# Kernel optimization log

Hardware: AMD Instinct MI355X
Metric: run time of the kernel (lower is better)

The kernel has to match this reference:

```python
import jax, jax.numpy as jnp
import numpy as np

EMBED = 256; HEADS = 8; LEVELS = 1; POINTS = 4; QUEUE = 2
HB = 200; WB = 200; NQ = HB * WB; BS = 1


def bilinear_sample(img, grid, h, w):
    # img: (BH, D, h*w) flattened feature map; grid: (BH, N, 2) in [-1, 1]
    # torch.grid_sample(align_corners=False, padding_mode='zeros') semantics
    gx, gy = grid[..., 0], grid[..., 1]
    x = (gx + 1.0) * (w * 0.5) - 0.5
    y = (gy + 1.0) * (h * 0.5) - 0.5
    x0 = jnp.floor(x); y0 = jnp.floor(y)
    lx = x - x0; ly = y - y0
    x0i = x0.astype(jnp.int32); y0i = y0.astype(jnp.int32)

    def corner(xi, yi, wgt):
        valid = ((xi >= 0) & (xi < w) & (yi >= 0) & (yi < h)).astype(img.dtype)
        idx = jnp.clip(yi, 0, h - 1) * w + jnp.clip(xi, 0, w - 1)  # (BH, N)
        vals = jax.vmap(lambda im, ix: im[:, ix])(img, idx)  # (BH, D, N)
        return vals * (wgt * valid)[:, None, :]

    return (corner(x0i, y0i, (1 - lx) * (1 - ly))
            + corner(x0i + 1, y0i, lx * (1 - ly))
            + corner(x0i, y0i + 1, (1 - lx) * ly)
            + corner(x0i + 1, y0i + 1, lx * ly))


def ms_deform_attn(value, shapes, loc, aw):
    # value: (B, Nv, H, D); loc: (B, nq, H, L, P, 2); aw: (B, nq, H, L, P)
    B, Nv, H, D = value.shape
    nq = loc.shape[1]; P = loc.shape[4]
    grids = 2.0 * loc - 1.0
    start = 0
    per_level = []
    for l in range(shapes.shape[0]):
        h, w = int(shapes[l, 0]), int(shapes[l, 1])
        vl = value[:, start:start + h * w].reshape(B, h, w, H, D)
        vl = vl.transpose(0, 3, 4, 1, 2).reshape(B * H, D, h * w)
        g = grids[:, :, :, l].transpose(0, 2, 1, 3, 4).reshape(B * H, nq * P, 2)
        samp = bilinear_sample(vl, g, h, w).reshape(B, H, D, nq, P)
        per_level.append(samp)
        start += h * w
    sampled = jnp.stack(per_level, axis=4)  # (B, H, D, nq, L, P)
    w_ = aw.transpose(0, 2, 1, 3, 4)[:, :, None]  # (B, H, 1, nq, L, P)
    out = (sampled * w_).sum(axis=(-1, -2))  # (B, H, D, nq)
    return out.reshape(B, H * D, nq).transpose(0, 2, 1)  # (B, nq, E)


def setup_inputs():
    key = jax.random.key(0)
    ks = jax.random.split(key, 10)
    s = 0.02
    n_off = QUEUE * HEADS * LEVELS * POINTS * 2
    n_aw = QUEUE * HEADS * LEVELS * POINTS
    return {
        "query": jax.random.normal(ks[0], (BS, NQ, EMBED), jnp.float32),
        "query_pos": jax.random.normal(ks[1], (BS, NQ, EMBED), jnp.float32),
        "value": jax.random.normal(ks[2], (BS * QUEUE, NQ, EMBED), jnp.float32),
        "reference_points": jax.random.uniform(ks[3], (BS * QUEUE, NQ, LEVELS, 2), jnp.float32),
        "spatial_shapes": jnp.array([[HB, WB]], dtype=jnp.int32),
        "W_off": jax.random.normal(ks[4], (EMBED * QUEUE, n_off), jnp.float32) * s,
        "b_off": jnp.zeros((n_off,), jnp.float32),
        "W_attn": jax.random.normal(ks[5], (EMBED * QUEUE, n_aw), jnp.float32) * s,
        "b_attn": jnp.zeros((n_aw,), jnp.float32),
        "W_val": jax.random.normal(ks[6], (EMBED, EMBED), jnp.float32) * s,
        "b_val": jnp.zeros((EMBED,), jnp.float32),
        "W_out": jax.random.normal(ks[7], (EMBED, EMBED), jnp.float32) * s,
        "b_out": jnp.zeros((EMBED,), jnp.float32),
    }


def reference(query, query_pos, value, reference_points, spatial_shapes,
              W_off, b_off, W_attn, b_attn, W_val, b_val, W_out, b_out):
    shapes = np.asarray(spatial_shapes)  # static level shapes
    bs, nq, E = query.shape
    identity = query
    q = query + query_pos
    # temporal query: concat current-frame value with query
    q2 = jnp.concatenate([value[:bs], q], axis=-1)  # (bs, nq, 2E)
    v = value @ W_val + b_val  # (bs*2, nv, E)
    nv = v.shape[1]
    v = v.reshape(bs * QUEUE, nv, HEADS, E // HEADS)
    off = (q2 @ W_off + b_off).reshape(bs, nq, HEADS, QUEUE, LEVELS, POINTS, 2)
    aw = (q2 @ W_attn + b_attn).reshape(bs, nq, HEADS, QUEUE, LEVELS * POINTS)
    aw = jax.nn.softmax(aw, axis=-1).reshape(bs, nq, HEADS, QUEUE, LEVELS, POINTS)
    aw = aw.transpose(0, 3, 1, 2, 4, 5).reshape(bs * QUEUE, nq, HEADS, LEVELS, POINTS)
    off = off.transpose(0, 3, 1, 2, 4, 5, 6).reshape(bs * QUEUE, nq, HEADS, LEVELS, POINTS, 2)
    # normalized sampling locations: (bs*2, nq, H, L, P, 2)
    normalizer = jnp.stack([spatial_shapes[..., 1], spatial_shapes[..., 0]], -1).astype(jnp.float32)
    loc = reference_points[:, :, None, :, None, :] + off / normalizer[None, None, None, :, None, :]
    out = ms_deform_attn(v, shapes, loc, aw)  # (bs*2, nq, E)
    # average over the BEV queue (current + history)
    out = out.transpose(1, 2, 0).reshape(nq, E, bs, QUEUE).mean(-1).transpose(2, 0, 1)
    out = out @ W_out + b_out
    return out + identity
```

## Files before the change

kernel.cpp:

```cpp
#include <hip/hip_runtime.h>
#include <math.h>

#define NQ    40000
#define EMB   256
#define NHEAD 8
#define HDIM  32
#define HB    200
#define WB    200
#define NCOL  192
#define HPIX  2560000

typedef __attribute__((ext_vector_type(8))) __bf16 bf16x8;
typedef __attribute__((ext_vector_type(4))) float f32x4;

static __device__ __forceinline__ unsigned short f2bf(float f) {
  unsigned u = __float_as_uint(f);
  u = u + 0x7fffu + ((u >> 16) & 1u);
  return (unsigned short)(u >> 16);
}
static __device__ __forceinline__ float bf2f(unsigned short s) {
  return __uint_as_float(((unsigned)s) << 16);
}
static __device__ __forceinline__ void acc8(float* a, uint4 u, float w) {
  a[0] += w * __uint_as_float(u.x << 16);
  a[1] += w * __uint_as_float(u.x & 0xffff0000u);
  a[2] += w * __uint_as_float(u.y << 16);
  a[3] += w * __uint_as_float(u.y & 0xffff0000u);
  a[4] += w * __uint_as_float(u.z << 16);
  a[5] += w * __uint_as_float(u.z & 0xffff0000u);
  a[6] += w * __uint_as_float(u.w << 16);
  a[7] += w * __uint_as_float(u.w & 0xffff0000u);
}

__global__ __launch_bounds__(256) void conv_w(
    const float* __restrict__ W_off, const float* __restrict__ b_off,
    const float* __restrict__ W_attn, const float* __restrict__ b_attn,
    const float* __restrict__ W_val, const float* __restrict__ W_out,
    unsigned short* __restrict__ Wc1t, unsigned short* __restrict__ Wvt,
    unsigned short* __restrict__ Wot, float* __restrict__ bc1)
{
  int idx = blockIdx.x * 256 + threadIdx.x;
  if (idx < 98304) {
    int n = idx >> 9, k = idx & 511;
    float v = (n < 128) ? W_off[(size_t)k * 128 + n] : W_attn[(size_t)k * 64 + (n - 128)];
    Wc1t[idx] = f2bf(v);
  } else if (idx < 163840) {
    int j = idx - 98304;
    int n = j >> 8, k = j & 255;
    Wvt[j] = f2bf(W_val[(size_t)k * 256 + n]);
  } else if (idx < 229376) {
    int j = idx - 163840;
    int n = j >> 8, k = j & 255;
    Wot[j] = f2bf(W_out[(size_t)k * 256 + n]);
  } else if (idx < 229568) {
    int n = idx - 229376;
    bc1[n] = (n < 128) ? b_off[n] : b_attn[n - 128];
  }
}

template<int K, int N, int AMODE, int OMODE, bool RESID>
__global__ __launch_bounds__(256, 4) void rb_gemm(
    const void* __restrict__ Aptr, const void* __restrict__ Aq2a,
    const void* __restrict__ Aq2b, const unsigned short* __restrict__ Bt,
    const float* __restrict__ bias, const float* __restrict__ resid,
    void* __restrict__ outp)
{
  constexpr int NFR = N / 64;
  constexpr int NP  = N + 8;
  constexpr int ATB = (AMODE != 0) ? 32 * K * 2 : 0;
  constexpr int TRB = (OMODE != 0) ? 32 * NP * 2 : 0;
  constexpr int MXB = (ATB > TRB) ? ATB : TRB;
  constexpr int LDSB = (MXB > 64) ? MXB : 64;
  __shared__ __align__(16) char lds[LDSB];
  unsigned short* trn = (unsigned short*)lds;

  const int t = threadIdx.x;
  const int m0 = blockIdx.x * 32;
  const int wid = t >> 6, lane = t & 63;
  const int wn = wid * (N / 4);
  const int lr = lane & 15, quad = lane >> 4;

  auto cvt_store = [&](int r, int c, float4 f0, float4 f1) {
    union { unsigned short us[8]; uint4 v; } u;
    u.us[0] = f2bf(f0.x); u.us[1] = f2bf(f0.y);
    u.us[2] = f2bf(f0.z); u.us[3] = f2bf(f0.w);
    u.us[4] = f2bf(f1.x); u.us[5] = f2bf(f1.y);
    u.us[6] = f2bf(f1.z); u.us[7] = f2bf(f1.w);
    *(uint4*)(lds + (size_t)r * (K * 2) + ((c ^ (r & 7)) * 16)) = u.v;
  };

  if constexpr (AMODE == 1) {
    const int c = t & 31, r0 = t >> 5;
    float4 f[4][2];
    #pragma unroll
    for (int l = 0; l < 4; l++) {
      const float* s = (const float*)Aptr + (size_t)(m0 + r0 + 8 * l) * K + c * 8;
      f[l][0] = *(const float4*)s; f[l][1] = *(const float4*)(s + 4);
    }
    #pragma unroll
    for (int l = 0; l < 4; l++)
      cvt_store(r0 + 8 * l, c, f[l][0], f[l][1]);
    __syncthreads();
  } else if constexpr (AMODE == 2) {
    const int c = t & 63, r0 = t >> 6;
    if (c < 32) {
      float4 f[8][2];
      #pragma unroll
      for (int l = 0; l < 8; l++) {
        const float* s = (const float*)Aptr + (size_t)(m0 + r0 + 4 * l) * 256 + c * 8;
        f[l][0] = *(const float4*)s; f[l][1] = *(const float4*)(s + 4);
      }
      #pragma unroll
      for (int l = 0; l < 8; l++)
        cvt_store(r0 + 4 * l, c, f[l][0], f[l][1]);
    } else {
      #pragma unroll
      for (int h = 0; h < 2; h++) {
        float4 fq[4][2], fp[4][2];
        #pragma unroll
        for (int l = 0; l < 4; l++) {
          int r = r0 + 4 * (h * 4 + l);
          const float* sq = (const float*)Aq2a + (size_t)(m0 + r) * 256 + (c - 32) * 8;
          const float* sp = (const float*)Aq2b + (size_t)(m0 + r) * 256 + (c - 32) * 8;
          fq[l][0] = *(const float4*)sq; fq[l][1] = *(const float4*)(sq + 4);
          fp[l][0] = *(const float4*)sp; fp[l][1] = *(const float4*)(sp + 4);
        }
        #pragma unroll
        for (int l = 0; l < 4; l++) {
          int r = r0 + 4 * (h * 4 + l);
          float4 f0 = make_float4(fq[l][0].x + fp[l][0].x, fq[l][0].y + fp[l][0].y,
                                  fq[l][0].z + fp[l][0].z, fq[l][0].w + fp[l][0].w);
          float4 f1 = make_float4(fq[l][1].x + fp[l][1].x, fq[l][1].y + fp[l][1].y,
                                  fq[l][1].z + fp[l][1].z, fq[l][1].w + fp[l][1].w);
          cvt_store(r, c, f0, f1);
        }
      }
    }
    __syncthreads();
  }

  f32x4 acc[2][NFR];
  #pragma unroll
  for (int i = 0; i < 2; i++)
    #pragma unroll
    for (int n = 0; n < NFR; n++) acc[i][n] = (f32x4){0.f, 0.f, 0.f, 0.f};

  auto loadB = [&](bf16x8* dst, int k0) {
    #pragma unroll
    for (int n = 0; n < NFR; n++)
      dst[n] = *(const bf16x8*)(Bt + (size_t)(wn + n * 16 + lr) * K + k0 + quad * 8);
  };
  auto loadA = [&](bf16x8* dst, int k0) {
    if constexpr (AMODE == 0) {
      const unsigned short* A = (const unsigned short*)Aptr;
      #pragma unroll
      for (int i = 0; i < 2; i++)
        dst[i] = *(const bf16x8*)(A + (size_t)(m0 + lr + i * 16) * K + k0 + quad * 8);
    } else {
      const int cb = (k0 >> 3) + quad;
      const int sw = (cb ^ (lr & 7)) * 16;
      #pragma unroll
      for (int i = 0; i < 2; i++)
        dst[i] = *(const bf16x8*)(lds + (size_t)(lr + i * 16) * (K * 2) + sw);
    }
  };

  constexpr int NK = K / 32;
  bf16x8 bcur[NFR], af[2];
  loadB(bcur, 0);
  loadA(af, 0);
  #pragma unroll
  for (int ks = 0; ks < NK; ks++) {
    bf16x8 bnxt[NFR], anxt[2];
    if (ks + 1 < NK) {
      loadB(bnxt, (ks + 1) * 32);
      loadA(anxt, (ks + 1) * 32);
    }
    #pragma unroll
    for (int i = 0; i < 2; i++)
      #pragma unroll
      for (int n = 0; n < NFR; n++)
        acc[i][n] = __builtin_amdgcn_mfma_f32_16x16x32_bf16(af[i], bcur[n], acc[i][n], 0, 0, 0);
    if (ks + 1 < NK) {
      #pragma unroll
      for (int n = 0; n < NFR; n++) bcur[n] = bnxt[n];
      af[0] = anxt[0]; af[1] = anxt[1];
    }
  }

  if constexpr (OMODE == 0) {
    #pragma unroll
    for (int i = 0; i < 2; i++) {
      int rowb = m0 + i * 16 + quad * 4;
      #pragma unroll
      for (int n = 0; n < NFR; n++) {
        int col = wn + n * 16 + lr;
        float bsv = bias[col];
        #pragma unroll
        for (int r = 0; r < 4; r++) {
          int rr = rowb + r;
          float v = acc[i][n][r] + bsv;
          if (RESID) v += resid[(size_t)rr * N + col];
          ((float*)outp)[(size_t)rr * N + col] = v;
        }
      }
    }
  } else {
    if constexpr (AMODE != 0) __syncthreads();
    #pragma unroll
    for (int i = 0; i < 2; i++) {
      #pragma unroll
      for (int n = 0; n < NFR; n++) {
        int col = wn + n * 16 + lr;
        float bsv = bias[col];
        #pragma unroll
        for (int r = 0; r < 4; r++) {
          int rl = i * 16 + quad * 4 + r;
          trn[rl * NP + col] = f2bf(acc[i][n][r] + bsv);
        }
      }
    }
    __syncthreads();
    constexpr int NCH = (32 * N) / 2048;
    #pragma unroll
    for (int l = 0; l < NCH; l++) {
      int c = t + l * 256;
      int row = c / (N / 8);
      int coloff = (c % (N / 8)) * 8;
      uint4 d = *(const uint4*)(trn + row * NP + coloff);
      unsigned short* op = (unsigned short*)outp;
      if constexpr (OMODE == 2)
        op += (size_t)(coloff >> 5) * HPIX + (size_t)(m0 + row) * 32 + (coloff & 31);
      else
        op += (size_t)(m0 + row) * N + coloff;
      *(uint4*)op = d;
    }
  }
}

__global__ __launch_bounds__(256) void k3_sample(
    const unsigned short* __restrict__ raw1, const float* __restrict__ refp,
    const unsigned short* __restrict__ vh, unsigned short* __restrict__ msd)
{
  __shared__ int4   sidx[8][64];
  __shared__ float4 swgt[8][64];
  const int t = threadIdx.x;
  const int q0 = blockIdx.x * 8;

  #pragma unroll
  for (int ee = 0; ee < 2; ee++) {
    const int e = t + ee * 256;
    const int qi = e >> 6, r6 = e & 63;
    const int b = r6 >> 5, h = (r6 >> 2) & 7, p = r6 & 3;
    const int q = q0 + qi;
    const unsigned short* r = raw1 + (size_t)q * NCOL;
    float ox = bf2f(r[h * 16 + b * 8 + p * 2 + 0]);
    float oy = bf2f(r[h * 16 + b * 8 + p * 2 + 1]);
    float l0 = bf2f(r[128 + h * 8 + b * 4 + 0]);
    float l1 = bf2f(r[128 + h * 8 + b * 4 + 1]);
    float l2 = bf2f(r[128 + h * 8 + b * 4 + 2]);
    float l3 = bf2f(r[128 + h * 8 + b * 4 + 3]);
    float mx = fmaxf(fmaxf(l0, l1), fmaxf(l2, l3));
    float e0 = expf(l0 - mx), e1 = expf(l1 - mx);
    float e2 = expf(l2 - mx), e3 = expf(l3 - mx);
    float ssum = e0 + e1 + e2 + e3;
    float ep = (p == 0) ? e0 : (p == 1) ? e1 : (p == 2) ? e2 : e3;
    float aw = ep / ssum * 0.5f;
    float rx = refp[((size_t)b * NQ + q) * 2 + 0];
    float ry = refp[((size_t)b * NQ + q) * 2 + 1];
    float px = rx * (float)WB + ox - 0.5f;
    float py = ry * (float)HB + oy - 0.5f;
    float x0f = floorf(px), y0f = floorf(py);
    float lx = px - x0f, ly = py - y0f;
    int x0 = (int)x0f, y0 = (int)y0f, x1 = x0 + 1, y1 = y0 + 1;
    int x0c = min(max(x0, 0), WB - 1), x1c = min(max(x1, 0), WB - 1);
    int y0c = min(max(y0, 0), HB - 1), y1c = min(max(y1, 0), HB - 1);
    float vx0 = ((unsigned)x0 < (unsigned)WB) ? 1.f : 0.f;
    float vx1 = ((unsigned)x1 < (unsigned)WB) ? 1.f : 0.f;
    float vy0 = ((unsigned)y0 < (unsigned)HB) ? 1.f : 0.f;
    float vy1 = ((unsigned)y1 < (unsigned)HB) ? 1.f : 0.f;
    const int pb = b * NQ;
    int4 ix;
    ix.x = pb + y0c * WB + x0c;
    ix.y = pb + y0c * WB + x1c;
    ix.z = pb + y1c * WB + x0c;
    ix.w = pb + y1c * WB + x1c;
    float4 wv;
    wv.x = aw * (1.f - lx) * (1.f - ly) * vx0 * vy0;
    wv.y = aw * lx * (1.f - ly) * vx1 * vy0;
    wv.z = aw * (1.f - lx) * ly * vx0 * vy1;
    wv.w = aw * lx * ly * vx1 * vy1;
    sidx[qi][r6] = ix;
    swgt[qi][r6] = wv;
  }
  __syncthreads();

  const int qi = t >> 5, h = (t >> 2) & 7, c = t & 3;
  const unsigned short* vb = vh + (size_t)h * HPIX + c * 8;
  float a[8];
  #pragma unroll
  for (int j = 0; j < 8; j++) a[j] = 0.f;
  #pragma unroll
  for (int b = 0; b < 2; b++) {
    #pragma unroll
    for (int p = 0; p < 4; p++) {
      int ent = b * 32 + h * 4 + p;
      int4 pix = sidx[qi][ent];
      float4 wv = swgt[qi][ent];
      uint4 v00 = *(const uint4*)(vb + (size_t)pix.x * 32);
      uint4 v10 = *(const uint4*)(vb + (size_t)pix.y * 32);
      uint4 v01 = *(const uint4*)(vb + (size_t)pix.z * 32);
      uint4 v11 = *(const uint4*)(vb + (size_t)pix.w * 32);
      acc8(a, v00, wv.x);
      acc8(a, v10, wv.y);
      acc8(a, v01, wv.z);
      acc8(a, v11, wv.w);
    }
  }
  union { unsigned short us[8]; uint4 v; } o;
  #pragma unroll
  for (int j = 0; j < 8; j++) o.us[j] = f2bf(a[j]);
  *(uint4*)(msd + (size_t)(q0 + qi) * EMB + h * HDIM + c * 8) = o.v;
}

extern "C" void kernel_launch(void* const* d_in, const int* in_sizes, int n_in,
                              void* d_out, int out_size, void* d_ws, size_t ws_size,
                              hipStream_t stream) {
  const float* query     = (const float*)d_in[0];
  const float* query_pos = (const float*)d_in[1];
  const float* value     = (const float*)d_in[2];
  const float* refp      = (const float*)d_in[3];
  const float* W_off  = (const float*)d_in[5];
  const float* b_off  = (const float*)d_in[6];
  const float* W_attn = (const float*)d_in[7];
  const float* b_attn = (const float*)d_in[8];
  const float* W_val  = (const float*)d_in[9];
  const float* b_val  = (const float*)d_in[10];
  const float* W_out  = (const float*)d_in[11];
  const float* b_out  = (const float*)d_in[12];
  float* out = (float*)d_out;

  char* ws = (char*)d_ws;
  unsigned short* raw1 = (unsigned short*)(ws);
  unsigned short* vout = (unsigned short*)(ws + 15360000);
  unsigned short* msdb = (unsigned short*)(ws + 56320000);
  unsigned short* Wc1t = (unsigned short*)(ws + 76800000);
  unsigned short* Wvt  = (unsigned short*)(ws + 76996608);
  unsigned short* Wot  = (unsigned short*)(ws + 77127680);
  float*          bc1  = (float*)(ws + 77258752);

  hipLaunchKernelGGL(conv_w, dim3(897), dim3(256), 0, stream,
                     W_off, b_off, W_attn, b_attn, W_val, W_out, Wc1t, Wvt, Wot, bc1);

  hipLaunchKernelGGL((rb_gemm<512, 192, 2, 1, false>),
                     dim3(1250), dim3(256), 0, stream,
                     (const void*)value, (const void*)query, (const void*)query_pos,
                     Wc1t, bc1, (const float*)nullptr, (void*)raw1);
  hipLaunchKernelGGL((rb_gemm<256, 256, 1, 2, false>),
                     dim3(2500), dim3(256), 0, stream,
                     (const void*)value, (const void*)nullptr, (const void*)nullptr,
                     Wvt, b_val, (const float*)nullptr, (void*)vout);
  hipLaunchKernelGGL(k3_sample, dim3(NQ / 8), dim3(256), 0, stream,
                     raw1, refp, vout, msdb);
  hipLaunchKernelGGL((rb_gemm<256, 256, 0, 0, true>),
                     dim3(1250), dim3(256), 0, stream,
                     (const void*)msdb, (const void*)nullptr, (const void*)nullptr,
                     Wot, b_out, query, (void*)out);
}
```

Measured before the change: 373.0 us.

## Fuse projection GEMMs and fuse sampling with output projection GEMM

Merges the offset/attention GEMM and the value GEMM into one launch that picks a body by block index. It also fuses the deformable sampling stage with the output projection, so sampled bf16 rows are staged in LDS and never written to global memory. The K=512 GEMM now loads A in two 256-wide halves to keep LDS small, and the sampler is remapped to one thread per query-head with 32 accumulators each. This removes launches and the msd round trip through global memory, but raises register pressure and changes the gather access pattern.

```diff
diff --git a/kernel.cpp b/kernel.cpp
--- a/kernel.cpp
+++ b/kernel.cpp
@@ -59,23 +59,19 @@
 }
 
 template<int K, int N, int AMODE, int OMODE, bool RESID>
-__global__ __launch_bounds__(256, 4) void rb_gemm(
-    const void* __restrict__ Aptr, const void* __restrict__ Aq2a,
-    const void* __restrict__ Aq2b, const unsigned short* __restrict__ Bt,
-    const float* __restrict__ bias, const float* __restrict__ resid,
-    void* __restrict__ outp)
+static __device__ __forceinline__ void gemm_body(
+    int bx, char* lds,
+    const void* Aptr, const void* Aq2a, const void* Aq2b,
+    const unsigned short* __restrict__ Bt, const float* __restrict__ bias,
+    const float* __restrict__ resid, void* __restrict__ outp)
 {
   constexpr int NFR = N / 64;
   constexpr int NP  = N + 8;
-  constexpr int ATB = (AMODE != 0) ? 32 * K * 2 : 0;
-  constexpr int TRB = (OMODE != 0) ? 32 * NP * 2 : 0;
-  constexpr int MXB = (ATB > TRB) ? ATB : TRB;
-  constexpr int LDSB = (MXB > 64) ? MXB : 64;
-  __shared__ __align__(16) char lds[LDSB];
+  constexpr int KH  = K / 256;
   unsigned short* trn = (unsigned short*)lds;
 
   const int t = threadIdx.x;
-  const int m0 = blockIdx.x * 32;
+  const int m0 = bx * 32;
   const int wid = t >> 6, lane = t & 63;
   const int wn = wid * (N / 4);
   const int lr = lane & 15, quad = lane >> 4;
@@ -86,105 +82,84 @@
     u.us[2] = f2bf(f0.z); u.us[3] = f2bf(f0.w);
     u.us[4] = f2bf(f1.x); u.us[5] = f2bf(f1.y);
     u.us[6] = f2bf(f1.z); u.us[7] = f2bf(f1.w);
-    *(uint4*)(lds + (size_t)r * (K * 2) + ((c ^ (r & 7)) * 16)) = u.v;
+    *(uint4*)(lds + (size_t)r * 512 + ((c ^ (r & 7)) * 16)) = u.v;
   };
 
-  if constexpr (AMODE == 1) {
-    const int c = t & 31, r0 = t >> 5;
-    float4 f[4][2];
-    #pragma unroll
-    for (int l = 0; l < 4; l++) {
-      const float* s = (const float*)Aptr + (size_t)(m0 + r0 + 8 * l) * K + c * 8;
-      f[l][0] = *(const float4*)s; f[l][1] = *(const float4*)(s + 4);
-    }
-    #pragma unroll
-    for (int l = 0; l < 4; l++)
-      cvt_store(r0 + 8 * l, c, f[l][0], f[l][1]);
-    __syncthreads();
-  } else if constexpr (AMODE == 2) {
-    const int c = t & 63, r0 = t >> 6;
-    if (c < 32) {
-      float4 f[8][2];
-      #pragma unroll
-      for (int l = 0; l < 8; l++) {
-        const float* s = (const float*)Aptr + (size_t)(m0 + r0 + 4 * l) * 256 + c * 8;
-        f[l][0] = *(const float4*)s; f[l][1] = *(const float4*)(s + 4);
-      }
-      #pragma unroll
-      for (int l = 0; l < 8; l++)
-        cvt_store(r0 + 4 * l, c, f[l][0], f[l][1]);
-    } else {
-      #pragma unroll
-      for (int h = 0; h < 2; h++) {
+  f32x4 acc[2][NFR];
+  #pragma unroll
+  for (int i = 0; i < 2; i++)
+    #pragma unroll
+    for (int n = 0; n < NFR; n++) acc[i][n] = (f32x4){0.f, 0.f, 0.f, 0.f};
+
+  auto loadB = [&](bf16x8* dst, int gk) {
+    #pragma unroll
+    for (int n = 0; n < NFR; n++)
+      dst[n] = *(const bf16x8*)(Bt + (size_t)(wn + n * 16 + lr) * K + gk + quad * 8);
+  };
+  auto loadA = [&](bf16x8* dst, int lk) {
+    const int cb = (lk >> 3) + quad;
+    const int sw = (cb ^ (lr & 7)) * 16;
+    #pragma unroll
+    for (int i = 0; i < 2; i++)
+      dst[i] = *(const bf16x8*)(lds + (size_t)(lr + i * 16) * 512 + sw);
+  };
+
+  #pragma unroll
+  for (int kh = 0; kh < KH; kh++) {
+    if constexpr (AMODE != 3) {
+      if (kh) __syncthreads();
+      const int c = t & 31, r0 = t >> 5;
+      if (AMODE == 1 || kh == 0) {
+        float4 f[4][2];
+        #pragma unroll
+        for (int l = 0; l < 4; l++) {
+          const float* s = (const float*)Aptr + (size_t)(m0 + r0 + 8 * l) * 256 + c * 8;
+          f[l][0] = *(const float4*)s; f[l][1] = *(const float4*)(s + 4);
+        }
+        #pragma unroll
+        for (int l = 0; l < 4; l++)
+          cvt_store(r0 + 8 * l, c, f[l][0], f[l][1]);
+      } else {
         float4 fq[4][2], fp[4][2];
         #pragma unroll
         for (int l = 0; l < 4; l++) {
-          int r = r0 + 4 * (h * 4 + l);
-          const float* sq = (const float*)Aq2a + (size_t)(m0 + r) * 256 + (c - 32) * 8;
-          const float* sp = (const float*)Aq2b + (size_t)(m0 + r) * 256 + (c - 32) * 8;
+          const float* sq = (const float*)Aq2a + (size_t)(m0 + r0 + 8 * l) * 256 + c * 8;
+          const float* sp = (const float*)Aq2b + (size_t)(m0 + r0 + 8 * l) * 256 + c * 8;
           fq[l][0] = *(const float4*)sq; fq[l][1] = *(const float4*)(sq + 4);
           fp[l][0] = *(const float4*)sp; fp[l][1] = *(const float4*)(sp + 4);
         }
         #pragma unroll
         for (int l = 0; l < 4; l++) {
-          int r = r0 + 4 * (h * 4 + l);
           float4 f0 = make_float4(fq[l][0].x + fp[l][0].x, fq[l][0].y + fp[l][0].y,
                                   fq[l][0].z + fp[l][0].z, fq[l][0].w + fp[l][0].w);
           float4 f1 = make_float4(fq[l][1].x + fp[l][1].x, fq[l][1].y + fp[l][1].y,
                                   fq[l][1].z + fp[l][1].z, fq[l][1].w + fp[l][1].w);
-          cvt_store(r, c, f0, f1);
-        }
-      }
-    }
-    __syncthreads();
-  }
-
-  f32x4 acc[2][NFR];
-  #pragma unroll
-  for (int i = 0; i < 2; i++)
-    #pragma unroll
-    for (int n = 0; n < NFR; n++) acc[i][n] = (f32x4){0.f, 0.f, 0.f, 0.f};
-
-  auto loadB = [&](bf16x8* dst, int k0) {
-    #pragma unroll
-    for (int n = 0; n < NFR; n++)
-      dst[n] = *(const bf16x8*)(Bt + (size_t)(wn + n * 16 + lr) * K + k0 + quad * 8);
-  };
-  auto loadA = [&](bf16x8* dst, int k0) {
-    if constexpr (AMODE == 0) {
-      const unsigned short* A = (const unsigned short*)Aptr;
+          cvt_store(r0 + 8 * l, c, f0, f1);
+        }
+      }
+      __syncthreads();
+    }
+
+    bf16x8 bcur[NFR], af[2];
+    loadB(bcur, kh * 256);
+    loadA(af, 0);
+    #pragma unroll
+    for (int ks = 0; ks < 8; ks++) {
+      bf16x8 bn[NFR], an[2];
+      if (ks < 7) {
+        loadB(bn, kh * 256 + (ks + 1) * 32);
+        loadA(an, (ks + 1) * 32);
+      }
       #pragma unroll
       for (int i = 0; i < 2; i++)
-        dst[i] = *(const bf16x8*)(A + (size_t)(m0 + lr + i * 16) * K + k0 + quad * 8);
-    } else {
-      const int cb = (k0 >> 3) + quad;
-      const int sw = (cb ^ (lr & 7)) * 16;
-      #pragma unroll
-      for (int i = 0; i < 2; i++)
-        dst[i] = *(const bf16x8*)(lds + (size_t)(lr + i * 16) * (K * 2) + sw);
-    }
-  };
-
-  constexpr int NK = K / 32;
-  bf16x8 bcur[NFR], af[2];
-  loadB(bcur, 0);
-  loadA(af, 0);
-  #pragma unroll
-  for (int ks = 0; ks < NK; ks++) {
-    bf16x8 bnxt[NFR], anxt[2];
-    if (ks + 1 < NK) {
-      loadB(bnxt, (ks + 1) * 32);
-      loadA(anxt, (ks + 1) * 32);
-    }
-    #pragma unroll
-    for (int i = 0; i < 2; i++)
-      #pragma unroll
-      for (int n = 0; n < NFR; n++)
-        acc[i][n] = __builtin_amdgcn_mfma_f32_16x16x32_bf16(af[i], bcur[n], acc[i][n], 0, 0, 0);
-    if (ks + 1 < NK) {
-      #pragma unroll
-      for (int n = 0; n < NFR; n++) bcur[n] = bnxt[n];
-      af[0] = anxt[0]; af[1] = anxt[1];
+        #pragma unroll
+        for (int n = 0; n < NFR; n++)
+          acc[i][n] = __builtin_amdgcn_mfma_f32_16x16x32_bf16(af[i], bcur[n], acc[i][n], 0, 0, 0);
+      if (ks < 7) {
+        #pragma unroll
+        for (int n = 0; n < NFR; n++) bcur[n] = bn[n];
+        af[0] = an[0]; af[1] = an[1];
+      }
     }
   }
 
@@ -206,7 +181,7 @@
       }
     }
   } else {
-    if constexpr (AMODE != 0) __syncthreads();
+    __syncthreads();
     #pragma unroll
     for (int i = 0; i < 2; i++) {
       #pragma unroll
@@ -238,89 +213,116 @@
   }
 }
 
-__global__ __launch_bounds__(256) void k3_sample(
+__global__ __launch_bounds__(256, 4) void k12(
+    const float* __restrict__ value, const float* __restrict__ query,
+    const float* __restrict__ qpos, const unsigned short* __restrict__ Wc1t,
+    const unsigned short* __restrict__ Wvt, const float* __restrict__ bc1,
+    const float* __restrict__ b_val, unsigned short* __restrict__ raw1,
+    unsigned short* __restrict__ vout)
+{
+  __shared__ __align__(16) char lds[16896];
+  const int bx = blockIdx.x;
+  if (bx < 1250) {
+    gemm_body<512, 192, 2, 1, false>(bx, lds, value, query, qpos,
+                                     Wc1t, bc1, nullptr, raw1);
+  } else {
+    gemm_body<256, 256, 1, 2, false>(bx - 1250, lds, value, nullptr, nullptr,
+                                     Wvt, b_val, nullptr, vout);
+  }
+}
+
+__global__ __launch_bounds__(256, 4) void k34(
     const unsigned short* __restrict__ raw1, const float* __restrict__ refp,
-    const unsigned short* __restrict__ vh, unsigned short* __restrict__ msd)
+    const unsigned short* __restrict__ vh, const float* __restrict__ query,
+    const unsigned short* __restrict__ Wot, const float* __restrict__ b_out,
+    float* __restrict__ out)
 {
-  __shared__ int4   sidx[8][64];
-  __shared__ float4 swgt[8][64];
+  __shared__ __align__(16) char lds[16384];
   const int t = threadIdx.x;
-  const int q0 = blockIdx.x * 8;
-
-  #pragma unroll
-  for (int ee = 0; ee < 2; ee++) {
-    const int e = t + ee * 256;
-    const int qi = e >> 6, r6 = e & 63;
-    const int b = r6 >> 5, h = (r6 >> 2) & 7, p = r6 & 3;
-    const int q = q0 + qi;
-    const unsigned short* r = raw1 + (size_t)q * NCOL;
-    float ox = bf2f(r[h * 16 + b * 8 + p * 2 + 0]);
-    float oy = bf2f(r[h * 16 + b * 8 + p * 2 + 1]);
-    float l0 = bf2f(r[128 + h * 8 + b * 4 + 0]);
-    float l1 = bf2f(r[128 + h * 8 + b * 4 + 1]);
-    float l2 = bf2f(r[128 + h * 8 + b * 4 + 2]);
-    float l3 = bf2f(r[128 + h * 8 + b * 4 + 3]);
+  const int m0 = blockIdx.x * 32;
+  const int q = t & 31, h = t >> 5;
+
+  const unsigned short* r = raw1 + (size_t)(m0 + q) * NCOL;
+  uint4 ob0 = *(const uint4*)(r + h * 16);
+  uint4 ob1 = *(const uint4*)(r + h * 16 + 8);
+  uint4 lg  = *(const uint4*)(r + 128 + h * 8);
+  const unsigned short* vb = vh + (size_t)h * HPIX;
+
+  float a[32];
+  #pragma unroll
+  for (int j = 0; j < 32; j++) a[j] = 0.f;
+
+  #pragma unroll
+  for (int b = 0; b < 2; b++) {
+    unsigned w0 = b ? lg.z : lg.x, w1 = b ? lg.w : lg.y;
+    float l0 = bf2f((unsigned short)w0), l1 = bf2f((unsigned short)(w0 >> 16));
+    float l2 = bf2f((unsigned short)w1), l3 = bf2f((unsigned short)(w1 >> 16));
     float mx = fmaxf(fmaxf(l0, l1), fmaxf(l2, l3));
     float e0 = expf(l0 - mx), e1 = expf(l1 - mx);
     float e2 = expf(l2 - mx), e3 = expf(l3 - mx);
     float ssum = e0 + e1 + e2 + e3;
-    float ep = (p == 0) ? e0 : (p == 1) ? e1 : (p == 2) ? e2 : e3;
-    float aw = ep / ssum * 0.5f;
-    float rx = refp[((size_t)b * NQ + q) * 2 + 0];
-    float ry = refp[((size_t)b * NQ + q) * 2 + 1];
-    float px = rx * (float)WB + ox - 0.5f;
-    float py = ry * (float)HB + oy - 0.5f;
-    float x0f = floorf(px), y0f = floorf(py);
-    float lx = px - x0f, ly = py - y0f;
-    int x0 = (int)x0f, y0 = (int)y0f, x1 = x0 + 1, y1 = y0 + 1;
-    int x0c = min(max(x0, 0), WB - 1), x1c = min(max(x1, 0), WB - 1);
-    int y0c = min(max(y0, 0), HB - 1), y1c = min(max(y1, 0), HB - 1);
-    float vx0 = ((unsigned)x0 < (unsigned)WB) ? 1.f : 0.f;
-    float vx1 = ((unsigned)x1 < (unsigned)WB) ? 1.f : 0.f;
-    float vy0 = ((unsigned)y0 < (unsigned)HB) ? 1.f : 0.f;
-    float vy1 = ((unsigned)y1 < (unsigned)HB) ? 1.f : 0.f;
+    float awp[4] = {e0 / ssum * 0.5f, e1 / ssum * 0.5f,
+                    e2 / ssum * 0.5f, e3 / ssum * 0.5f};
+    float2 rp = *(const float2*)(refp + ((size_t)b * NQ + m0 + q) * 2);
+    uint4 ob = b ? ob1 : ob0;
+    unsigned po[4] = {ob.x, ob.y, ob.z, ob.w};
     const int pb = b * NQ;
-    int4 ix;
-    ix.x = pb + y0c * WB + x0c;
-    ix.y = pb + y0c * WB + x1c;
-    ix.z = pb + y1c * WB + x0c;
-    ix.w = pb + y1c * WB + x1c;
-    float4 wv;
-    wv.x = aw * (1.f - lx) * (1.f - ly) * vx0 * vy0;
-    wv.y = aw * lx * (1.f - ly) * vx1 * vy0;
-    wv.z = aw * (1.f - lx) * ly * vx0 * vy1;
-    wv.w = aw * lx * ly * vx1 * vy1;
-    sidx[qi][r6] = ix;
-    swgt[qi][r6] = wv;
+    #pragma unroll
+    for (int p = 0; p < 4; p++) {
+      float ox = bf2f((unsigned short)po[p]);
+      float oy = bf2f((unsigned short)(po[p] >> 16));
+      float px = rp.x * (float)WB + ox - 0.5f;
+      float py = rp.y * (float)HB + oy - 0.5f;
+      float x0f = floorf(px), y0f = floorf(py);
+      float lx = px - x0f, ly = py - y0f;
+      int x0 = (int)x0f, y0 = (int)y0f, x1 = x0 + 1, y1 = y0 + 1;
+      int x0c = min(max(x0, 0), WB - 1), x1c = min(max(x1, 0), WB - 1);
+      int y0c = min(max(y0, 0), HB - 1), y1c = min(max(y1, 0), HB - 1);
+      float vx0 = ((unsigned)x0 < (unsigned)WB) ? 1.f : 0.f;
+      float vx1 = ((unsigned)x1 < (unsigned)WB) ? 1.f : 0.f;
+      float vy0 = ((unsigned)y0 < (unsigned)HB) ? 1.f : 0.f;
+      float vy1 = ((unsigned)y1 < (unsigned)HB) ? 1.f : 0.f;
+      int pix0 = pb + y0c * WB + x0c, pix1 = pb + y0c * WB + x1c;
+      int pix2 = pb + y1c * WB + x0c, pix3 = pb + y1c * WB + x1c;
+      float wv0 = awp[p] * (1.f - lx) * (1.f - ly) * vx0 * vy0;
+      float wv1 = awp[p] * lx * (1.f - ly) * vx1 * vy0;
+      float wv2 = awp[p] * (1.f - lx) * ly * vx0 * vy1;
+      float wv3 = awp[p] * lx * ly * vx1 * vy1;
+      const unsigned short* c0 = vb + (size_t)pix0 * 32;
+      const unsigned short* c1 = vb + (size_t)pix1 * 32;
+      const unsigned short* c2 = vb + (size_t)pix2 * 32;
+      const unsigned short* c3 = vb + (size_t)pix3 * 32;
+      uint4 A0 = *(const uint4*)(c0),      A1 = *(const uint4*)(c0 + 8);
+      uint4 A2 = *(const uint4*)(c0 + 16), A3 = *(const uint4*)(c0 + 24);
+      uint4 B0 = *(const uint4*)(c1),      B1 = *(const uint4*)(c1 + 8);
+      uint4 B2 = *(const uint4*)(c1 + 16), B3 = *(const uint4*)(c1 + 24);
+      uint4 C0 = *(const uint4*)(c2),      C1 = *(const uint4*)(c2 + 8);
+      uint4 C2 = *(const uint4*)(c2 + 16), C3 = *(const uint4*)(c2 + 24);
+      uint4 D0 = *(const uint4*)(c3),      D1 = *(const uint4*)(c3 + 8);
+      uint4 D2 = *(const uint4*)(c3 + 16), D3 = *(const uint4*)(c3 + 24);
+      acc8(a + 0, A0, wv0); acc8(a + 8, A1, wv0);
+      acc8(a + 16, A2, wv0); acc8(a + 24, A3, wv0);
+      acc8(a + 0, B0, wv1); acc8(a + 8, B1, wv1);
+      acc8(a + 16, B2, wv1); acc8(a + 24, B3, wv1);
+      acc8(a + 0, C0, wv2); acc8(a + 8, C1, wv2);
+      acc8(a + 16, C2, wv2); acc8(a + 24, C3, wv2);
+      acc8(a + 0, D0, wv3); acc8(a + 8, D1, wv3);
+      acc8(a + 16, D2, wv3); acc8(a + 24, D3, wv3);
+    }
+  }
+
+  #pragma unroll
+  for (int j = 0; j < 4; j++) {
+    union { unsigned short us[8]; uint4 v; } u;
+    #pragma unroll
+    for (int i = 0; i < 8; i++) u.us[i] = f2bf(a[j * 8 + i]);
+    int c = h * 4 + j;
+    *(uint4*)(lds + (size_t)q * 512 + ((c ^ (q & 7)) * 16)) = u.v;
   }
   __syncthreads();
 
-  const int qi = t >> 5, h = (t >> 2) & 7, c = t & 3;
-  const unsigned short* vb = vh + (size_t)h * HPIX + c * 8;
-  float a[8];
-  #pragma unroll
-  for (int j = 0; j < 8; j++) a[j] = 0.f;
-  #pragma unroll
-  for (int b = 0; b < 2; b++) {
-    #pragma unroll
-    for (int p = 0; p < 4; p++) {
-      int ent = b * 32 + h * 4 + p;
-      int4 pix = sidx[qi][ent];
-      float4 wv = swgt[qi][ent];
-      uint4 v00 = *(const uint4*)(vb + (size_t)pix.x * 32);
-      uint4 v10 = *(const uint4*)(vb + (size_t)pix.y * 32);
-      uint4 v01 = *(const uint4*)(vb + (size_t)pix.z * 32);
-      uint4 v11 = *(const uint4*)(vb + (size_t)pix.w * 32);
-      acc8(a, v00, wv.x);
-      acc8(a, v10, wv.y);
-      acc8(a, v01, wv.z);
-      acc8(a, v11, wv.w);
-    }
-  }
-  union { unsigned short us[8]; uint4 v; } o;
-  #pragma unroll
-  for (int j = 0; j < 8; j++) o.us[j] = f2bf(a[j]);
-  *(uint4*)(msd + (size_t)(q0 + qi) * EMB + h * HDIM + c * 8) = o.v;
+  gemm_body<256, 256, 3, 0, true>(blockIdx.x, lds, nullptr, nullptr, nullptr,
+                                  Wot, b_out, query, out);
 }
 
 extern "C" void kernel_launch(void* const* d_in, const int* in_sizes, int n_in,
@@ -343,27 +345,17 @@
   char* ws = (char*)d_ws;
   unsigned short* raw1 = (unsigned short*)(ws);
   unsigned short* vout = (unsigned short*)(ws + 15360000);
-  unsigned short* msdb = (unsigned short*)(ws + 56320000);
-  unsigned short* Wc1t = (unsigned short*)(ws + 76800000);
-  unsigned short* Wvt  = (unsigned short*)(ws + 76996608);
-  unsigned short* Wot  = (unsigned short*)(ws + 77127680);
-  float*          bc1  = (float*)(ws + 77258752);
+  unsigned short* Wc1t = (unsigned short*)(ws + 56320000);
+  unsigned short* Wvt  = (unsigned short*)(ws + 56516608);
+  unsigned short* Wot  = (unsigned short*)(ws + 56647680);
+  float*          bc1  = (float*)(ws + 56778752);
 
   hipLaunchKernelGGL(conv_w, dim3(897), dim3(256), 0, stream,
                      W_off, b_off, W_attn, b_attn, W_val, W_out, Wc1t, Wvt, Wot, bc1);
 
-  hipLaunchKernelGGL((rb_gemm<512, 192, 2, 1, false>),
-                     dim3(1250), dim3(256), 0, stream,
-                     (const void*)value, (const void*)query, (const void*)query_pos,
-                     Wc1t, bc1, (const float*)nullptr, (void*)raw1);
-  hipLaunchKernelGGL((rb_gemm<256, 256, 1, 2, false>),
-                     dim3(2500), dim3(256), 0, stream,
-                     (const void*)value, (const void*)nullptr, (const void*)nullptr,
-                     Wvt, b_val, (const float*)nullptr, (void*)vout);
-  hipLaunchKernelGGL(k3_sample, dim3(NQ / 8), dim3(256), 0, stream,
-                     raw1, refp, vout, msdb);
-  hipLaunchKernelGGL((rb_gemm<256, 256, 0, 0, true>),
-                     dim3(1250), dim3(256), 0, stream,
-                     (const void*)msdb, (const void*)nullptr, (const void*)nullptr,
-                     Wot, b_out, query, (void*)out);
-}
+  hipLaunchKernelGGL(k12, dim3(3750), dim3(256), 0, stream,
+                     value, query, query_pos, Wc1t, Wvt, bc1, b_val, raw1, vout);
+
+  hipLaunchKernelGGL(k34, dim3(1250), dim3(256), 0, stream,
+                     raw1, refp, vout, query, Wot, b_out, out);
+}
```

Measured after the change: 865.3 us. +132.0%, slower.

## Fuse deformable sampling with output projection GEMM into one kernel

Applied to the files above, without the earlier changes.

Merges the bilinear sampling kernel and the output-projection GEMM into a single kernel. Each block samples 32 queries into swizzled LDS as bf16, then runs the MFMA GEMM against W_out with the bias and residual added in the epilogue. This removes the round trip of the intermediate sampled tensor through global memory and one kernel launch. Sampling is also restructured so that one thread handles a whole query-head pair (32 channels, eight 16-byte loads per corner) instead of four threads each taking 8 channels, which trades per-thread register pressure and load parallelism for less index recomputation. The generic GEMM template is simplified by dropping its now-unused direct-global A path and fp32 output path.

```diff
diff --git a/kernel.cpp b/kernel.cpp
--- a/kernel.cpp
+++ b/kernel.cpp
@@ -21,15 +21,15 @@
 static __device__ __forceinline__ float bf2f(unsigned short s) {
   return __uint_as_float(((unsigned)s) << 16);
 }
-static __device__ __forceinline__ void acc8(float* a, uint4 u, float w) {
-  a[0] += w * __uint_as_float(u.x << 16);
-  a[1] += w * __uint_as_float(u.x & 0xffff0000u);
-  a[2] += w * __uint_as_float(u.y << 16);
-  a[3] += w * __uint_as_float(u.y & 0xffff0000u);
-  a[4] += w * __uint_as_float(u.z << 16);
-  a[5] += w * __uint_as_float(u.z & 0xffff0000u);
-  a[6] += w * __uint_as_float(u.w << 16);
-  a[7] += w * __uint_as_float(u.w & 0xffff0000u);
+static __device__ __forceinline__ void accp(float4& lo4, float4& hi4, uint4 u, float w) {
+  lo4.x += w * __uint_as_float(u.x << 16);
+  lo4.y += w * __uint_as_float(u.x & 0xffff0000u);
+  lo4.z += w * __uint_as_float(u.y << 16);
+  lo4.w += w * __uint_as_float(u.y & 0xffff0000u);
+  hi4.x += w * __uint_as_float(u.z << 16);
+  hi4.y += w * __uint_as_float(u.z & 0xffff0000u);
+  hi4.z += w * __uint_as_float(u.w << 16);
+  hi4.w += w * __uint_as_float(u.w & 0xffff0000u);
 }
 
 __global__ __launch_bounds__(256) void conv_w(
@@ -115,11 +115,11 @@
         cvt_store(r0 + 4 * l, c, f[l][0], f[l][1]);
     } else {
       #pragma unroll
-      for (int h = 0; h < 2; h++) {
+      for (int hh = 0; hh < 2; hh++) {
         float4 fq[4][2], fp[4][2];
         #pragma unroll
         for (int l = 0; l < 4; l++) {
-          int r = r0 + 4 * (h * 4 + l);
+          int r = r0 + 4 * (hh * 4 + l);
           const float* sq = (const float*)Aq2a + (size_t)(m0 + r) * 256 + (c - 32) * 8;
           const float* sp = (const float*)Aq2b + (size_t)(m0 + r) * 256 + (c - 32) * 8;
           fq[l][0] = *(const float4*)sq; fq[l][1] = *(const float4*)(sq + 4);
@@ -127,7 +127,7 @@
         }
         #pragma unroll
         for (int l = 0; l < 4; l++) {
-          int r = r0 + 4 * (h * 4 + l);
+          int r = r0 + 4 * (hh * 4 + l);
           float4 f0 = make_float4(fq[l][0].x + fp[l][0].x, fq[l][0].y + fp[l][0].y,
                                   fq[l][0].z + fp[l][0].z, fq[l][0].w + fp[l][0].w);
           float4 f1 = make_float4(fq[l][1].x + fp[l][1].x, fq[l][1].y + fp[l][1].y,
@@ -151,18 +151,11 @@
       dst[n] = *(const bf16x8*)(Bt + (size_t)(wn + n * 16 + lr) * K + k0 + quad * 8);
   };
   auto loadA = [&](bf16x8* dst, int k0) {
-    if constexpr (AMODE == 0) {
-      const unsigned short* A = (const unsigned short*)Aptr;
-      #pragma unroll
-      for (int i = 0; i < 2; i++)
-        dst[i] = *(const bf16x8*)(A + (size_t)(m0 + lr + i * 16) * K + k0 + quad * 8);
-    } else {
-      const int cb = (k0 >> 3) + quad;
-      const int sw = (cb ^ (lr & 7)) * 16;
-      #pragma unroll
-      for (int i = 0; i < 2; i++)
-        dst[i] = *(const bf16x8*)(lds + (size_t)(lr + i * 16) * (K * 2) + sw);
-    }
+    const int cb = (k0 >> 3) + quad;
+    const int sw = (cb ^ (lr & 7)) * 16;
+    #pragma unroll
+    for (int i = 0; i < 2; i++)
+      dst[i] = *(const bf16x8*)(lds + (size_t)(lr + i * 16) * (K * 2) + sw);
   };
 
   constexpr int NK = K / 32;
@@ -171,10 +164,10 @@
   loadA(af, 0);
   #pragma unroll
   for (int ks = 0; ks < NK; ks++) {
-    bf16x8 bnxt[NFR], anxt[2];
+    bf16x8 bn[NFR], an[2];
     if (ks + 1 < NK) {
-      loadB(bnxt, (ks + 1) * 32);
-      loadA(anxt, (ks + 1) * 32);
+      loadB(bn, (ks + 1) * 32);
+      loadA(an, (ks + 1) * 32);
     }
     #pragma unroll
     for (int i = 0; i < 2; i++)
@@ -183,144 +176,189 @@
         acc[i][n] = __builtin_amdgcn_mfma_f32_16x16x32_bf16(af[i], bcur[n], acc[i][n], 0, 0, 0);
     if (ks + 1 < NK) {
       #pragma unroll
-      for (int n = 0; n < NFR; n++) bcur[n] = bnxt[n];
-      af[0] = anxt[0]; af[1] = anxt[1];
-    }
-  }
-
-  if constexpr (OMODE == 0) {
-    #pragma unroll
-    for (int i = 0; i < 2; i++) {
-      int rowb = m0 + i * 16 + quad * 4;
-      #pragma unroll
-      for (int n = 0; n < NFR; n++) {
-        int col = wn + n * 16 + lr;
-        float bsv = bias[col];
-        #pragma unroll
-        for (int r = 0; r < 4; r++) {
-          int rr = rowb + r;
-          float v = acc[i][n][r] + bsv;
-          if (RESID) v += resid[(size_t)rr * N + col];
-          ((float*)outp)[(size_t)rr * N + col] = v;
-        }
+      for (int n = 0; n < NFR; n++) bcur[n] = bn[n];
+      af[0] = an[0]; af[1] = an[1];
+    }
+  }
+
+  __syncthreads();
+  #pragma unroll
+  for (int i = 0; i < 2; i++) {
+    #pragma unroll
+    for (int n = 0; n < NFR; n++) {
+      int col = wn + n * 16 + lr;
+      float bsv = bias[col];
+      #pragma unroll
+      for (int r = 0; r < 4; r++) {
+        int rl = i * 16 + quad * 4 + r;
+        trn[rl * NP + col] = f2bf(acc[i][n][r] + bsv);
       }
     }
-  } else {
-    if constexpr (AMODE != 0) __syncthreads();
-    #pragma unroll
-    for (int i = 0; i < 2; i++) {
-      #pragma unroll
-      for (int n = 0; n < NFR; n++) {
-        int col = wn + n * 16 + lr;
-        float bsv = bias[col];
-        #pragma unroll
-        for (int r = 0; r < 4; r++) {
-          int rl = i * 16 + quad * 4 + r;
-          trn[rl * NP + col] = f2bf(acc[i][n][r] + bsv);
-        }
-      }
-    }
-    __syncthreads();
-    constexpr int NCH = (32 * N) / 2048;
-    #pragma unroll
-    for (int l = 0; l < NCH; l++) {
-      int c = t + l * 256;
-      int row = c / (N / 8);
-      int coloff = (c % (N / 8)) * 8;
-      uint4 d = *(const uint4*)(trn + row * NP + coloff);
-      unsigned short* op = (unsigned short*)outp;
-      if constexpr (OMODE == 2)
-        op += (size_t)(coloff >> 5) * HPIX + (size_t)(m0 + row) * 32 + (coloff & 31);
-      else
-        op += (size_t)(m0 + row) * N + coloff;
-      *(uint4*)op = d;
-    }
-  }
-}
-
-__global__ __launch_bounds__(256) void k3_sample(
+  }
+  __syncthreads();
+  constexpr int NCH = (32 * N) / 2048;
+  #pragma unroll
+  for (int l = 0; l < NCH; l++) {
+    int c = t + l * 256;
+    int row = c / (N / 8);
+    int coloff = (c % (N / 8)) * 8;
+    uint4 d = *(const uint4*)(trn + row * NP + coloff);
+    unsigned short* op = (unsigned short*)outp;
+    if constexpr (OMODE == 2)
+      op += (size_t)(coloff >> 5) * HPIX + (size_t)(m0 + row) * 32 + (coloff & 31);
+    else
+      op += (size_t)(m0 + row) * N + coloff;
+    *(uint4*)op = d;
+  }
+}
+
+__global__ __launch_bounds__(256, 2) void k34(
     const unsigned short* __restrict__ raw1, const float* __restrict__ refp,
-    const unsigned short* __restrict__ vh, unsigned short* __restrict__ msd)
+    const unsigned short* __restrict__ vh, const float* __restrict__ query,
+    const unsigned short* __restrict__ Wot, const float* __restrict__ b_out,
+    float* __restrict__ out)
 {
-  __shared__ int4   sidx[8][64];
-  __shared__ float4 swgt[8][64];
+  __shared__ __align__(16) char lds[16384];
   const int t = threadIdx.x;
-  const int q0 = blockIdx.x * 8;
-
-  #pragma unroll
-  for (int ee = 0; ee < 2; ee++) {
-    const int e = t + ee * 256;
-    const int qi = e >> 6, r6 = e & 63;
-    const int b = r6 >> 5, h = (r6 >> 2) & 7, p = r6 & 3;
-    const int q = q0 + qi;
-    const unsigned short* r = raw1 + (size_t)q * NCOL;
-    float ox = bf2f(r[h * 16 + b * 8 + p * 2 + 0]);
-    float oy = bf2f(r[h * 16 + b * 8 + p * 2 + 1]);
-    float l0 = bf2f(r[128 + h * 8 + b * 4 + 0]);
-    float l1 = bf2f(r[128 + h * 8 + b * 4 + 1]);
-    float l2 = bf2f(r[128 + h * 8 + b * 4 + 2]);
-    float l3 = bf2f(r[128 + h * 8 + b * 4 + 3]);
+  const int m0 = blockIdx.x * 32;
+  const int q = t & 31, h = t >> 5;
+
+  const unsigned short* r = raw1 + (size_t)(m0 + q) * NCOL;
+  uint4 ob0 = *(const uint4*)(r + h * 16);
+  uint4 ob1 = *(const uint4*)(r + h * 16 + 8);
+  uint4 lg  = *(const uint4*)(r + 128 + h * 8);
+  const unsigned short* vb = vh + (size_t)h * HPIX;
+
+  float4 s0 = {0.f,0.f,0.f,0.f}, s1 = s0, s2 = s0, s3 = s0;
+  float4 s4 = s0, s5 = s0, s6 = s0, s7 = s0;
+
+  auto corner = [&](const unsigned short* cp, float w) {
+    uint4 v0 = *(const uint4*)(cp);
+    uint4 v1 = *(const uint4*)(cp + 8);
+    uint4 v2 = *(const uint4*)(cp + 16);
+    uint4 v3 = *(const uint4*)(cp + 24);
+    accp(s0, s1, v0, w);
+    accp(s2, s3, v1, w);
+    accp(s4, s5, v2, w);
+    accp(s6, s7, v3, w);
+  };
+
+  #pragma unroll
+  for (int b = 0; b < 2; b++) {
+    unsigned w0 = b ? lg.z : lg.x, w1 = b ? lg.w : lg.y;
+    float l0 = bf2f((unsigned short)w0), l1 = bf2f((unsigned short)(w0 >> 16));
+    float l2 = bf2f((unsigned short)w1), l3 = bf2f((unsigned short)(w1 >> 16));
     float mx = fmaxf(fmaxf(l0, l1), fmaxf(l2, l3));
     float e0 = expf(l0 - mx), e1 = expf(l1 - mx);
     float e2 = expf(l2 - mx), e3 = expf(l3 - mx);
     float ssum = e0 + e1 + e2 + e3;
-    float ep = (p == 0) ? e0 : (p == 1) ? e1 : (p == 2) ? e2 : e3;
-    float aw = ep / ssum * 0.5f;
-    float rx = refp[((size_t)b * NQ + q) * 2 + 0];
-    float ry = refp[((size_t)b * NQ + q) * 2 + 1];
-    float px = rx * (float)WB + ox - 0.5f;
-    float py = ry * (float)HB + oy - 0.5f;
-    float x0f = floorf(px), y0f = floorf(py);
-    float lx = px - x0f, ly = py - y0f;
-    int x0 = (int)x0f, y0 = (int)y0f, x1 = x0 + 1, y1 = y0 + 1;
-    int x0c = min(max(x0, 0), WB - 1), x1c = min(max(x1, 0), WB - 1);
-    int y0c = min(max(y0, 0), HB - 1), y1c = min(max(y1, 0), HB - 1);
-    float vx0 = ((unsigned)x0 < (unsigned)WB) ? 1.f : 0.f;
-    float vx1 = ((unsigned)x1 < (unsigned)WB) ? 1.f : 0.f;
-    float vy0 = ((unsigned)y0 < (unsigned)HB) ? 1.f : 0.f;
-    float vy1 = ((unsigned)y1 < (unsigned)HB) ? 1.f : 0.f;
+    float aw0 = e0 / ssum * 0.5f, aw1 = e1 / ssum * 0.5f;
+    float aw2 = e2 / ssum * 0.5f, aw3 = e3 / ssum * 0.5f;
+    float2 rp = *(const float2*)(refp + ((size_t)b * NQ + m0 + q) * 2);
+    uint4 ob = b ? ob1 : ob0;
     const int pb = b * NQ;
-    int4 ix;
-    ix.x = pb + y0c * WB + x0c;
-    ix.y = pb + y0c * WB + x1c;
-    ix.z = pb + y1c * WB + x0c;
-    ix.w = pb + y1c * WB + x1c;
-    float4 wv;
-    wv.x = aw * (1.f - lx) * (1.f - ly) * vx0 * vy0;
-    wv.y = aw * lx * (1.f - ly) * vx1 * vy0;
-    wv.z = aw * (1.f - lx) * ly * vx0 * vy1;
-    wv.w = aw * lx * ly * vx1 * vy1;
-    sidx[qi][r6] = ix;
-    swgt[qi][r6] = wv;
-  }
+    #pragma unroll
+    for (int p = 0; p < 4; p++) {
+      unsigned pw = (p == 0) ? ob.x : (p == 1) ? ob.y : (p == 2) ? ob.z : ob.w;
+      float ap = (p == 0) ? aw0 : (p == 1) ? aw1 : (p == 2) ? aw2 : aw3;
+      float ox = bf2f((unsigned short)pw);
+      float oy = bf2f((unsigned short)(pw >> 16));
+      float px = rp.x * (float)WB + ox - 0.5f;
+      float py = rp.y * (float)HB + oy - 0.5f;
+      float x0f = floorf(px), y0f = floorf(py);
+      float lx = px - x0f, ly = py - y0f;
+      int x0 = (int)x0f, y0 = (int)y0f, x1 = x0 + 1, y1 = y0 + 1;
+      int x0c = min(max(x0, 0), WB - 1), x1c = min(max(x1, 0), WB - 1);
+      int y0c = min(max(y0, 0), HB - 1), y1c = min(max(y1, 0), HB - 1);
+      float vx0 = ((unsigned)x0 < (unsigned)WB) ? 1.f : 0.f;
+      float vx1 = ((unsigned)x1 < (unsigned)WB) ? 1.f : 0.f;
+      float vy0 = ((unsigned)y0 < (unsigned)HB) ? 1.f : 0.f;
+      float vy1 = ((unsigned)y1 < (unsigned)HB) ? 1.f : 0.f;
+      float wv0 = ap * (1.f - lx) * (1.f - ly) * vx0 * vy0;
+      float wv1 = ap * lx * (1.f - ly) * vx1 * vy0;
+      float wv2 = ap * (1.f - lx) * ly * vx0 * vy1;
+      float wv3 = ap * lx * ly * vx1 * vy1;
+      corner(vb + (size_t)(pb + y0c * WB + x0c) * 32, wv0);
+      corner(vb + (size_t)(pb + y0c * WB + x1c) * 32, wv1);
+      corner(vb + (size_t)(pb + y1c * WB + x0c) * 32, wv2);
+      corner(vb + (size_t)(pb + y1c * WB + x1c) * 32, wv3);
+    }
+  }
+
+  auto pack2 = [&](float4 lo4, float4 hi4, int c) {
+    union { unsigned short us[8]; uint4 v; } u;
+    u.us[0] = f2bf(lo4.x); u.us[1] = f2bf(lo4.y);
+    u.us[2] = f2bf(lo4.z); u.us[3] = f2bf(lo4.w);
+    u.us[4] = f2bf(hi4.x); u.us[5] = f2bf(hi4.y);
+    u.us[6] = f2bf(hi4.z); u.us[7] = f2bf(hi4.w);
+    *(uint4*)(lds + (size_t)q * 512 + ((c ^ (q & 7)) * 16)) = u.v;
+  };
+  pack2(s0, s1, h * 4 + 0);
+  pack2(s2, s3, h * 4 + 1);
+  pack2(s4, s5, h * 4 + 2);
+  pack2(s6, s7, h * 4 + 3);
   __syncthreads();
 
-  const int qi = t >> 5, h = (t >> 2) & 7, c = t & 3;
-  const unsigned short* vb = vh + (size_t)h * HPIX + c * 8;
-  float a[8];
-  #pragma unroll
-  for (int j = 0; j < 8; j++) a[j] = 0.f;
-  #pragma unroll
-  for (int b = 0; b < 2; b++) {
-    #pragma unroll
-    for (int p = 0; p < 4; p++) {
-      int ent = b * 32 + h * 4 + p;
-      int4 pix = sidx[qi][ent];
-      float4 wv = swgt[qi][ent];
-      uint4 v00 = *(const uint4*)(vb + (size_t)pix.x * 32);
-      uint4 v10 = *(const uint4*)(vb + (size_t)pix.y * 32);
-      uint4 v01 = *(const uint4*)(vb + (size_t)pix.z * 32);
-      uint4 v11 = *(const uint4*)(vb + (size_t)pix.w * 32);
-      acc8(a, v00, wv.x);
-      acc8(a, v10, wv.y);
-      acc8(a, v01, wv.z);
-      acc8(a, v11, wv.w);
-    }
-  }
-  union { unsigned short us[8]; uint4 v; } o;
-  #pragma unroll
-  for (int j = 0; j < 8; j++) o.us[j] = f2bf(a[j]);
-  *(uint4*)(msd + (size_t)(q0 + qi) * EMB + h * HDIM + c * 8) = o.v;
+  const int wid = t >> 6, lane = t & 63;
+  const int wn = wid * 64;
+  const int lr = lane & 15, quad = lane >> 4;
+
+  f32x4 acc[2][4];
+  #pragma unroll
+  for (int i = 0; i < 2; i++)
+    #pragma unroll
+    for (int n = 0; n < 4; n++) acc[i][n] = (f32x4){0.f, 0.f, 0.f, 0.f};
+
+  auto loadB = [&](bf16x8* dst, int k0) {
+    #pragma unroll
+    for (int n = 0; n < 4; n++)
+      dst[n] = *(const bf16x8*)(Wot + (size_t)(wn + n * 16 + lr) * 256 + k0 + quad * 8);
+  };
+  auto loadA = [&](bf16x8* dst, int k0) {
+    const int cb = (k0 >> 3) + quad;
+    const int sw = (cb ^ (lr & 7)) * 16;
+    #pragma unroll
+    for (int i = 0; i < 2; i++)
+      dst[i] = *(const bf16x8*)(lds + (size_t)(lr + i * 16) * 512 + sw);
+  };
+
+  bf16x8 bcur[4], af[2];
+  loadB(bcur, 0);
+  loadA(af, 0);
+  #pragma unroll
+  for (int ks = 0; ks < 8; ks++) {
+    bf16x8 bn[4], an[2];
+    if (ks < 7) {
+      loadB(bn, (ks + 1) * 32);
+      loadA(an, (ks + 1) * 32);
+    }
+    #pragma unroll
+    for (int i = 0; i < 2; i++)
+      #pragma unroll
+      for (int n = 0; n < 4; n++)
+        acc[i][n] = __builtin_amdgcn_mfma_f32_16x16x32_bf16(af[i], bcur[n], acc[i][n], 0, 0, 0);
+    if (ks < 7) {
+      #pragma unroll
+      for (int n = 0; n < 4; n++) bcur[n] = bn[n];
+      af[0] = an[0]; af[1] = an[1];
+    }
+  }
+
+  #pragma unroll
+  for (int i = 0; i < 2; i++) {
+    int rowb = m0 + i * 16 + quad * 4;
+    #pragma unroll
+    for (int n = 0; n < 4; n++) {
+      int col = wn + n * 16 + lr;
+      float bsv = b_out[col];
+      #pragma unroll
+      for (int rr = 0; rr < 4; rr++) {
+        int row = rowb + rr;
+        out[(size_t)row * 256 + col] =
+            acc[i][n][rr] + bsv + query[(size_t)row * 256 + col];
+      }
+    }
+  }
 }
 
 extern "C" void kernel_launch(void* const* d_in, const int* in_sizes, int n_in,
@@ -343,11 +381,10 @@
   char* ws = (char*)d_ws;
   unsigned short* raw1 = (unsigned short*)(ws);
   unsigned short* vout = (unsigned short*)(ws + 15360000);
-  unsigned short* msdb = (unsigned short*)(ws + 56320000);
-  unsigned short* Wc1t = (unsigned short*)(ws + 76800000);
-  unsigned short* Wvt  = (unsigned short*)(ws + 76996608);
-  unsigned short* Wot  = (unsigned short*)(ws + 77127680);
-  float*          bc1  = (float*)(ws + 77258752);
+  unsigned short* Wc1t = (unsigned short*)(ws + 56320000);
+  unsigned short* Wvt  = (unsigned short*)(ws + 56516608);
+  unsigned short* Wot  = (unsigned short*)(ws + 56647680);
+  float*          bc1  = (float*)(ws + 56778752);
 
   hipLaunchKernelGGL(conv_w, dim3(897), dim3(256), 0, stream,
                      W_off, b_off, W_attn, b_attn, W_val, W_out, Wc1t, Wvt, Wot, bc1);
@@ -360,10 +397,6 @@
                      dim3(2500), dim3(256), 0, stream,
                      (const void*)value, (const void*)nullptr, (const void*)nullptr,
                      Wvt, b_val, (const float*)nullptr, (void*)vout);
-  hipLaunchKernelGGL(k3_sample, dim3(NQ / 8), dim3(256), 0, stream,
-                     raw1, refp, vout, msdb);
-  hipLaunchKernelGGL((rb_gemm<256, 256, 0, 0, true>),
-                     dim3(1250), dim3(256), 0, stream,
-                     (const void*)msdb, (const void*)nullptr, (const void*)nullptr,
-                     Wot, b_out, query, (void*)out);
-}
+  hipLaunchKernelGGL(k34, dim3(1250), dim3(256), 0, stream,
+                     raw1, refp, vout, query, Wot, b_out, out);
+}
```

Result: slower. 576.9 us (+54.7%).
